# Performance work log

Measured on AMD Instinct MI355X. Metric: run time of the kernel, lower is better.

Reference implementation:

```python
import jax, jax.numpy as jnp
import numpy as np

LN_EPS = 1e-5
KERNEL_EPS = 1e-4


def layer_norm(x, gamma, beta):
    mu = jnp.mean(x, axis=-1, keepdims=True)
    var = jnp.mean((x - mu) ** 2, axis=-1, keepdims=True)
    return (x - mu) * jax.lax.rsqrt(var + LN_EPS) * gamma + beta


def softmax_kernel(data, proj, is_query):
    # Performer softmax random-feature map (performer-pytorch softmax_kernel)
    d = data.shape[-1]
    m = proj.shape[0]
    data_normalizer = d ** -0.25
    ratio = m ** -0.5
    # [B,H,S,D] x [M,D] -> [B,H,S,M]
    proj_data = jnp.einsum('bhnd,md->bhnm', data_normalizer * data, proj)
    diag = 0.5 * (data_normalizer ** 2) * jnp.sum(data * data, axis=-1, keepdims=True)
    if is_query:
        mx = jax.lax.stop_gradient(jnp.max(proj_data, axis=-1, keepdims=True))
    else:
        mx = jax.lax.stop_gradient(jnp.max(proj_data, axis=(-2, -1), keepdims=True))
    return ratio * (jnp.exp(proj_data - diag - mx) + KERNEL_EPS)


def setup_inputs() -> dict:
    key = jax.random.key(0)
    k1, k2 = jax.random.split(key)
    B, S, D, M, H = 4, 4096, 256, 256, 8
    x = jax.random.normal(k1, (B, S, D), dtype=jnp.float32)
    gamma = jnp.ones((D,), dtype=jnp.float32)
    beta = jnp.zeros((D,), dtype=jnp.float32)
    proj_matrix = jax.random.normal(k2, (M, D), dtype=jnp.float32)
    return {"x": x, "gamma": gamma, "beta": beta, "proj_matrix": proj_matrix, "num_heads": H}


def reference(x, gamma, beta, proj_matrix, num_heads):
    xn = layer_norm(x, gamma, beta)                       # [B,S,D]
    B, S, D = xn.shape
    h = jnp.broadcast_to(xn[:, None], (B, num_heads, S, D))  # stacked copies per head
    q = softmax_kernel(h, proj_matrix, True)              # [B,H,S,M]
    k = softmax_kernel(h, proj_matrix, False)             # [B,H,S,M]
    v = h                                                 # [B,H,S,D]
    # non-causal linear attention
    k_sum = jnp.sum(k, axis=-2)                           # [B,H,M]
    d_inv = 1.0 / jnp.einsum('bhnm,bhm->bhn', q, k_sum)   # [B,H,S]
    context = jnp.einsum('bhnm,bhnd->bhmd', k, v)         # [B,H,M,D]
    out = jnp.einsum('bhmd,bhnm,bhn->bhnd', context, q, d_inv)
    return out
```

## Files before the change

kernel.cpp:

```cpp
#include <hip/hip_runtime.h>
#include <math.h>

#define Bn 4
#define Hn 8
#define Sn 4096
#define Dn 256
#define Mn 256
#define BSn (Bn*Sn)
#define LN_EPS 1e-5f
#define KEPS 1e-4f
#define DATA_NORM 0.25f
#define RATIO 0.0625f

typedef short s8v __attribute__((ext_vector_type(8)));
typedef short s4v __attribute__((ext_vector_type(4)));
typedef float f4v __attribute__((ext_vector_type(4)));

#define LSTR 40
#define BSTR 72

__device__ __forceinline__ unsigned short f2bf(float x) {
    unsigned u = __float_as_uint(x);
    u += 0x7FFFu + ((u >> 16) & 1u);
    return (unsigned short)(u >> 16);
}
__device__ __forceinline__ float bf2f(unsigned short h) {
    return __uint_as_float(((unsigned)h) << 16);
}
__device__ __forceinline__ unsigned enc_f(float f) {
    unsigned u = __float_as_uint(f);
    return (u & 0x80000000u) ? ~u : (u | 0x80000000u);
}
__device__ __forceinline__ float dec_f(unsigned u) {
    unsigned b = (u & 0x80000000u) ? (u ^ 0x80000000u) : ~u;
    return __uint_as_float(b);
}

__device__ __forceinline__ float blockReduceMax(float v) {
    __shared__ float buf[4];
    #pragma unroll
    for (int o = 32; o > 0; o >>= 1) v = fmaxf(v, __shfl_down(v, o));
    __syncthreads();
    if ((threadIdx.x & 63) == 0) buf[threadIdx.x >> 6] = v;
    __syncthreads();
    return fmaxf(fmaxf(buf[0], buf[1]), fmaxf(buf[2], buf[3]));
}

__device__ __forceinline__ void split8(const float* p, unsigned short* Lh,
                                       unsigned short* Ll, int off) {
    float v[8];
    *(float4*)&v[0] = *(const float4*)p;
    *(float4*)&v[4] = *(const float4*)(p + 4);
    s8v hh, ll;
    #pragma unroll
    for (int e = 0; e < 8; e++) {
        unsigned short h = f2bf(v[e]);
        hh[e] = (short)h;
        ll[e] = (short)f2bf(v[e] - bf2f(h));
    }
    *(s8v*)&Lh[off] = hh;
    *(s8v*)&Ll[off] = ll;
}

__device__ __forceinline__ void stage_tile(const float* base, int ld,
                                           unsigned short* Lh, unsigned short* Ll, int t) {
    const int row = t >> 1, c0 = (t & 1) * 16;
    const float* p = base + (size_t)row * ld + c0;
    split8(p,     Lh, Ll, row * LSTR + c0);
    split8(p + 8, Lh, Ll, row * LSTR + c0 + 8);
}

__device__ __forceinline__ void mfma_step(const unsigned short* Ah, const unsigned short* Al,
                                          const unsigned short* Bh, const unsigned short* Bl,
                                          int wr, int wc, int lane, f4v acc[4][4]) {
    s8v ah[4], al[4], bh[4], bl[4];
    const int quad = lane >> 4, r = lane & 15;
    #pragma unroll
    for (int i = 0; i < 4; i++) {
        const int m = wr * 64 + i * 16 + r;
        ah[i] = *(const s8v*)&Ah[m * LSTR + quad * 8];
        al[i] = *(const s8v*)&Al[m * LSTR + quad * 8];
        const int n = wc * 64 + i * 16 + r;
        bh[i] = *(const s8v*)&Bh[n * LSTR + quad * 8];
        bl[i] = *(const s8v*)&Bl[n * LSTR + quad * 8];
    }
    #pragma unroll
    for (int i = 0; i < 4; i++)
        #pragma unroll
        for (int j = 0; j < 4; j++) {
            acc[i][j] = __builtin_amdgcn_mfma_f32_16x16x32_bf16(ah[i], bh[j], acc[i][j], 0, 0, 0);
            acc[i][j] = __builtin_amdgcn_mfma_f32_16x16x32_bf16(ah[i], bl[j], acc[i][j], 0, 0, 0);
            acc[i][j] = __builtin_amdgcn_mfma_f32_16x16x32_bf16(al[i], bh[j], acc[i][j], 0, 0, 0);
        }
}

__device__ __forceinline__ void stage_bf16(const unsigned short* base, int ld,
                                           unsigned short* L, int t) {
    const int row = t >> 1, c0 = (t & 1) * 32;
    const unsigned short* p = base + (size_t)row * ld + c0;
    #pragma unroll
    for (int q = 0; q < 4; q++)
        *(s8v*)&L[row * BSTR + c0 + q * 8] = *(const s8v*)&p[q * 8];
}

__device__ __forceinline__ void mfma_step64(const unsigned short* A, const unsigned short* B,
                                            int wr, int wc, int lane, f4v acc[4][4]) {
    const int quad = lane >> 4, r = lane & 15;
    #pragma unroll
    for (int ks = 0; ks < 2; ks++) {
        s8v a[4], b[4];
        #pragma unroll
        for (int i = 0; i < 4; i++) {
            a[i] = *(const s8v*)&A[(wr * 64 + i * 16 + r) * BSTR + ks * 32 + quad * 8];
            b[i] = *(const s8v*)&B[(wc * 64 + i * 16 + r) * BSTR + ks * 32 + quad * 8];
        }
        #pragma unroll
        for (int i = 0; i < 4; i++)
            #pragma unroll
            for (int j = 0; j < 4; j++)
                acc[i][j] = __builtin_amdgcn_mfma_f32_16x16x32_bf16(a[i], b[j], acc[i][j], 0, 0, 0);
    }
}

__global__ __launch_bounds__(256) void k_ln(const float* __restrict__ X,
                                            const float* __restrict__ gamma,
                                            const float* __restrict__ beta,
                                            float* __restrict__ XN,
                                            float* __restrict__ diag,
                                            unsigned* __restrict__ mxqI) {
    const int w = threadIdx.x >> 6, l = threadIdx.x & 63;
    const int row = blockIdx.x * 4 + w;
    const float* p = X + (size_t)row * Dn + l * 4;
    float4 x = *(const float4*)p;
    float s = x.x + x.y + x.z + x.w;
    #pragma unroll
    for (int o = 32; o > 0; o >>= 1) s += __shfl_xor(s, o);
    const float mean = s * (1.0f / Dn);
    float4 v = make_float4(x.x - mean, x.y - mean, x.z - mean, x.w - mean);
    float vs = v.x * v.x + v.y * v.y + v.z * v.z + v.w * v.w;
    #pragma unroll
    for (int o = 32; o > 0; o >>= 1) vs += __shfl_xor(vs, o);
    const float rs = rsqrtf(vs * (1.0f / Dn) + LN_EPS);
    float4 g = *(const float4*)&gamma[l * 4];
    float4 bt = *(const float4*)&beta[l * 4];
    float4 xn = make_float4(v.x * rs * g.x + bt.x, v.y * rs * g.y + bt.y,
                            v.z * rs * g.z + bt.z, v.w * rs * g.w + bt.w);
    *(float4*)&XN[(size_t)row * Dn + l * 4] = xn;
    float d2 = xn.x * xn.x + xn.y * xn.y + xn.z * xn.z + xn.w * xn.w;
    #pragma unroll
    for (int o = 32; o > 0; o >>= 1) d2 += __shfl_xor(d2, o);
    if (l == 0) { diag[row] = 0.03125f * d2; mxqI[row] = 0u; }
}

__global__ __launch_bounds__(256, 2) void k_gemm1(const float* __restrict__ XN,
                                                  const float* __restrict__ P,
                                                  float* __restrict__ PD,
                                                  unsigned* __restrict__ mxqI) {
    __shared__ unsigned short Ah[128 * LSTR], Al[128 * LSTR];
    __shared__ unsigned short Bh[128 * LSTR], Bl[128 * LSTR];
    const int t = threadIdx.x, lane = t & 63, w = t >> 6;
    const int wr = w >> 1, wc = w & 1, quad = lane >> 4, cc = lane & 15;
    const int r0 = blockIdx.x * 128, m0 = blockIdx.y * 128;
    f4v acc[4][4];
    #pragma unroll
    for (int i = 0; i < 4; i++)
        #pragma unroll
        for (int j = 0; j < 4; j++)
            #pragma unroll
            for (int r = 0; r < 4; r++) acc[i][j][r] = 0.0f;

    for (int kt = 0; kt < Dn; kt += 32) {
        __syncthreads();
        stage_tile(XN + (size_t)r0 * Dn + kt, Dn, Ah, Al, t);
        stage_tile(P + (size_t)m0 * Dn + kt, Dn, Bh, Bl, t);
        __syncthreads();
        mfma_step(Ah, Al, Bh, Bl, wr, wc, lane, acc);
    }
    float rmax[4][4];
    #pragma unroll
    for (int i = 0; i < 4; i++)
        #pragma unroll
        for (int r = 0; r < 4; r++) rmax[i][r] = -INFINITY;
    #pragma unroll
    for (int i = 0; i < 4; i++) {
        const int row = r0 + wr * 64 + i * 16 + quad * 4;
        #pragma unroll
        for (int j = 0; j < 4; j++) {
            const int col = m0 + wc * 64 + j * 16 + cc;
            #pragma unroll
            for (int r = 0; r < 4; r++) {
                float v = DATA_NORM * acc[i][j][r];
                PD[(size_t)(row + r) * Mn + col] = v;
                rmax[i][r] = fmaxf(rmax[i][r], v);
            }
        }
    }
    #pragma unroll
    for (int i = 0; i < 4; i++)
        #pragma unroll
        for (int r = 0; r < 4; r++) {
            float v = rmax[i][r];
            v = fmaxf(v, __shfl_xor(v, 1));
            v = fmaxf(v, __shfl_xor(v, 2));
            v = fmaxf(v, __shfl_xor(v, 4));
            v = fmaxf(v, __shfl_xor(v, 8));
            if (cc == 0)
                atomicMax(&mxqI[r0 + wr * 64 + i * 16 + quad * 4 + r], enc_f(v));
        }
}

__global__ __launch_bounds__(256) void k_batchmax(const unsigned* __restrict__ mxqI,
                                                  float* __restrict__ mxqF,
                                                  float* __restrict__ mxk,
                                                  float* __restrict__ KSUM) {
    const int b = blockIdx.x;
    KSUM[b * Mn + threadIdx.x] = 0.0f;
    float m = -INFINITY;
    for (int i = threadIdx.x; i < Sn; i += 256) {
        float f = dec_f(mxqI[b * Sn + i]);
        mxqF[b * Sn + i] = f;
        m = fmaxf(m, f);
    }
    m = blockReduceMax(m);
    if (threadIdx.x == 0) mxk[b] = m;
}

__global__ __launch_bounds__(256) void k_featvt(const float* __restrict__ PD,
                                                const float* __restrict__ XN,
                                                const float* __restrict__ diag,
                                                const float* __restrict__ mxk,
                                                unsigned short* __restrict__ KT,
                                                unsigned short* __restrict__ VT,
                                                float* __restrict__ KSUM) {
    __shared__ float T[64][65];
    const int s0 = blockIdx.x * 64, c0 = blockIdx.y * 64;
    const int z = blockIdx.z;
    const int t = threadIdx.x;
    const int sr = t >> 2, cc = (t & 3) * 16;
    if (z < 4) {
        const int b = z;
        const int gr = b * Sn + s0 + sr;
        const float dmv = diag[gr] + mxk[b];
        const float* p = PD + (size_t)gr * Mn + c0 + cc;
        float v[16];
        *(float4*)&v[0]  = *(const float4*)&p[0];
        *(float4*)&v[4]  = *(const float4*)&p[4];
        *(float4*)&v[8]  = *(const float4*)&p[8];
        *(float4*)&v[12] = *(const float4*)&p[12];
        #pragma unroll
        for (int e = 0; e < 16; e++)
            T[cc + e][sr] = RATIO * (__expf(v[e] - dmv) + KEPS);
        __syncthreads();
        const int ml = t >> 2, sc = (t & 3) * 16;
        float ks = 0.0f;
        s8v o0, o1;
        #pragma unroll
        for (int i = 0; i < 8; i++) {
            float f0 = T[ml][sc + i], f1 = T[ml][sc + 8 + i];
            ks += f0 + f1;
            o0[i] = (short)f2bf(f0);
            o1[i] = (short)f2bf(f1);
        }
        unsigned short* q = KT + ((size_t)b * Mn + c0 + ml) * Sn + s0 + sc;
        *(s8v*)&q[0] = o0;
        *(s8v*)&q[8] = o1;
        ks += __shfl_xor(ks, 1);
        ks += __shfl_xor(ks, 2);
        if ((t & 3) == 0) atomicAdd(&KSUM[b * Mn + c0 + ml], ks);
    } else {
        const int b = z - 4;
        const int gr = b * Sn + s0 + sr;
        const float* p = XN + (size_t)gr * Dn + c0 + cc;
        float v[16];
        *(float4*)&v[0]  = *(const float4*)&p[0];
        *(float4*)&v[4]  = *(const float4*)&p[4];
        *(float4*)&v[8]  = *(const float4*)&p[8];
        *(float4*)&v[12] = *(const float4*)&p[12];
        #pragma unroll
        for (int e = 0; e < 16; e++) T[cc + e][sr] = v[e];
        __syncthreads();
        const int dl = t >> 2, sc = (t & 3) * 16;
        s8v o0, o1;
        #pragma unroll
        for (int i = 0; i < 8; i++) {
            o0[i] = (short)f2bf(T[dl][sc + i]);
            o1[i] = (short)f2bf(T[dl][sc + 8 + i]);
        }
        unsigned short* q = VT + ((size_t)b * Dn + c0 + dl) * Sn + s0 + sc;
        *(s8v*)&q[0] = o0;
        *(s8v*)&q[8] = o1;
    }
}

__global__ __launch_bounds__(256, 2) void k_gemm2(const unsigned short* __restrict__ VT,
                                                  const unsigned short* __restrict__ KT,
                                                  float* __restrict__ PART) {
    __shared__ unsigned short Abuf[128 * BSTR], Bbuf[128 * BSTR];
    const int t = threadIdx.x, lane = t & 63, w = t >> 6;
    const int wr = w >> 1, wc = w & 1, quad = lane >> 4, cc = lane & 15;
    const int chunk = blockIdx.x, til = blockIdx.y, b = blockIdx.z;
    const int d0 = (til >> 1) * 128, m0 = (til & 1) * 128;
    const unsigned short* Ab = VT + ((size_t)b * Dn + d0) * Sn + chunk * 256;
    const unsigned short* Bb = KT + ((size_t)b * Mn + m0) * Sn + chunk * 256;
    f4v acc[4][4];
    #pragma unroll
    for (int i = 0; i < 4; i++)
        #pragma unroll
        for (int j = 0; j < 4; j++)
            #pragma unroll
            for (int r = 0; r < 4; r++) acc[i][j][r] = 0.0f;

    for (int kt = 0; kt < 256; kt += 64) {
        __syncthreads();
        stage_bf16(Ab + kt, Sn, Abuf, t);
        stage_bf16(Bb + kt, Sn, Bbuf, t);
        __syncthreads();
        mfma_step64(Abuf, Bbuf, wr, wc, lane, acc);
    }
    float* dst = PART + (size_t)(chunk * Bn + b) * (Dn * Mn);
    #pragma unroll
    for (int i = 0; i < 4; i++) {
        const int drow = d0 + wr * 64 + i * 16 + quad * 4;
        #pragma unroll
        for (int j = 0; j < 4; j++) {
            const int col = m0 + wc * 64 + j * 16 + cc;
            #pragma unroll
            for (int r = 0; r < 4; r++)
                dst[(size_t)(drow + r) * Mn + col] = acc[i][j][r];
        }
    }
}

__global__ __launch_bounds__(256) void k_ctxred(const float* __restrict__ PART,
                                                unsigned short* __restrict__ CT) {
    const int g = blockIdx.x * 256 + threadIdx.x;
    float4 s = make_float4(0.f, 0.f, 0.f, 0.f);
    #pragma unroll
    for (int c = 0; c < 16; c++) {
        float4 p = *(const float4*)&PART[(size_t)c * 262144 + (size_t)g * 4];
        s.x += p.x; s.y += p.y; s.z += p.z; s.w += p.w;
    }
    s4v o;
    o[0] = (short)f2bf(s.x); o[1] = (short)f2bf(s.y);
    o[2] = (short)f2bf(s.z); o[3] = (short)f2bf(s.w);
    *(s4v*)&CT[(size_t)g * 4] = o;
}

__global__ __launch_bounds__(256, 2) void k_gemm3(const float* __restrict__ PD,
                                                  const unsigned short* __restrict__ CT,
                                                  const float* __restrict__ diag,
                                                  const float* __restrict__ mxqF,
                                                  const float* __restrict__ KSUM,
                                                  float* __restrict__ OUT) {
    __shared__ unsigned short Abuf[128 * BSTR], Bbuf[128 * BSTR];
    __shared__ float kslds[Mn];
    __shared__ float dinvS[128];
    const int t = threadIdx.x, lane = t & 63, w = t >> 6;
    const int wr = w >> 1, wc = w & 1, quad = lane >> 4, cc = lane & 15;
    const int r0 = blockIdx.x * 128, d0 = blockIdx.y * 128;
    const int b = r0 >> 12;
    kslds[t] = KSUM[b * Mn + t];
    const int arow = t >> 1, h = t & 1;
    const int gr = r0 + arow;
    const float dm = diag[gr] + mxqF[gr];
    const float* Ap = PD + (size_t)gr * Mn + h * 32;
    const unsigned short* Bb = CT + ((size_t)b * Dn + d0) * Mn;
    float qks = 0.0f;
    f4v acc[4][4];
    #pragma unroll
    for (int i = 0; i < 4; i++)
        #pragma unroll
        for (int j = 0; j < 4; j++)
            #pragma unroll
            for (int r = 0; r < 4; r++) acc[i][j][r] = 0.0f;

    for (int kt = 0; kt < Mn; kt += 64) {
        __syncthreads();
        {
            float v[32];
            #pragma unroll
            for (int q4 = 0; q4 < 8; q4++)
                *(float4*)&v[q4 * 4] = *(const float4*)&Ap[kt + q4 * 4];
            #pragma unroll
            for (int e = 0; e < 32; e++) {
                float qv = RATIO * (__expf(v[e] - dm) + KEPS);
                qks += qv * kslds[kt + h * 32 + e];
                v[e] = qv;
            }
            #pragma unroll
            for (int g8 = 0; g8 < 4; g8++) {
                s8v hh;
                #pragma unroll
                for (int e = 0; e < 8; e++) hh[e] = (short)f2bf(v[g8 * 8 + e]);
                *(s8v*)&Abuf[arow * BSTR + h * 32 + g8 * 8] = hh;
            }
        }
        stage_bf16(Bb + kt, Mn, Bbuf, t);
        __syncthreads();
        mfma_step64(Abuf, Bbuf, wr, wc, lane, acc);
    }
    qks += __shfl_xor(qks, 1);
    if (h == 0) dinvS[arow] = 1.0f / qks;
    __syncthreads();
    #pragma unroll
    for (int i = 0; i < 4; i++) {
        const int rl0 = wr * 64 + i * 16 + quad * 4;
        #pragma unroll
        for (int r = 0; r < 4; r++) {
            const int rl = rl0 + r;
            const int gr2 = r0 + rl;
            const float dv = dinvS[rl];
            const int ss = gr2 & (Sn - 1);
            const size_t base = ((size_t)(b * Hn) * Sn + ss) * Dn;
            #pragma unroll
            for (int j = 0; j < 4; j++) {
                const int col = d0 + wc * 64 + j * 16 + cc;
                const float val = acc[i][j][r] * dv;
                #pragma unroll
                for (int hh = 0; hh < Hn; hh++)
                    OUT[base + (size_t)hh * Sn * Dn + col] = val;
            }
        }
    }
}

extern "C" void kernel_launch(void* const* d_in, const int* in_sizes, int n_in,
                              void* d_out, int out_size, void* d_ws, size_t ws_size,
                              hipStream_t stream) {
    const float* X     = (const float*)d_in[0];
    const float* gamma = (const float*)d_in[1];
    const float* beta  = (const float*)d_in[2];
    const float* P     = (const float*)d_in[3];
    float* OUT = (float*)d_out;

    float* ws = (float*)d_ws;
    float* XN   = ws;
    float* PD   = XN + (size_t)4194304;
    float* diag = PD + (size_t)4194304;
    unsigned* mxqI = (unsigned*)(diag + 16384);
    float* mxqF = (float*)(mxqI + 16384);
    float* mxk  = mxqF + 16384;
    float* KSUM = mxk + 64;
    unsigned short* KT = (unsigned short*)(KSUM + 1024);
    unsigned short* VT = KT + (size_t)4194304;
    unsigned short* CT = VT + (size_t)4194304;
    float* PART = XN;

    k_ln<<<BSn / 4, 256, 0, stream>>>(X, gamma, beta, XN, diag, mxqI);
    k_gemm1<<<dim3(BSn / 128, Mn / 128), 256, 0, stream>>>(XN, P, PD, mxqI);
    k_batchmax<<<Bn, 256, 0, stream>>>(mxqI, mxqF, mxk, KSUM);
    k_featvt<<<dim3(Sn / 64, 4, 8), 256, 0, stream>>>(PD, XN, diag, mxk, KT, VT, KSUM);
    k_gemm2<<<dim3(16, 4, Bn), 256, 0, stream>>>(VT, KT, PART);
    k_ctxred<<<256, 256, 0, stream>>>(PART, CT);
    k_gemm3<<<dim3(BSn / 128, Dn / 128), 256, 0, stream>>>(PD, CT, diag, mxqF, KSUM, OUT);
}
```

Measured before the change: 221.6 us.

## Pre-split operands to bf16 hi/lo and precompute Q features in featvt

LayerNorm now writes bf16 hi/lo halves directly, and a new kernel pre-splits the projection matrix, so gemm1 stages bf16 tiles instead of converting fp32 per tile. Query features are computed once in featvt, rescaled from the key max, and stored as bf16, so gemm3 no longer re-reads fp32 PD and recomputes exp. Both GEMMs move to 64-row tiles with a 64-wide K step, and the workspace is repacked with KT aliasing XNl. The intent is to cut global traffic and redundant conversion and exp work. The cost is an extra launch, and Q is rescaled via exp(mxk-mxq) before bf16 rounding, which could affect accuracy.

```diff
diff --git a/kernel.cpp b/kernel.cpp
--- a/kernel.cpp
+++ b/kernel.cpp
@@ -16,7 +16,6 @@
 typedef short s4v __attribute__((ext_vector_type(4)));
 typedef float f4v __attribute__((ext_vector_type(4)));
 
-#define LSTR 40
 #define BSTR 72
 
 __device__ __forceinline__ unsigned short f2bf(float x) {
@@ -46,11 +45,41 @@
     return fmaxf(fmaxf(buf[0], buf[1]), fmaxf(buf[2], buf[3]));
 }
 
-__device__ __forceinline__ void split8(const float* p, unsigned short* Lh,
-                                       unsigned short* Ll, int off) {
+__device__ __forceinline__ void stage_bf16(const unsigned short* base, int ld,
+                                           unsigned short* L, int t) {
+    const int row = t >> 1, c0 = (t & 1) * 32;
+    const unsigned short* p = base + (size_t)row * ld + c0;
+    #pragma unroll
+    for (int q = 0; q < 4; q++)
+        *(s8v*)&L[row * BSTR + c0 + q * 8] = *(const s8v*)&p[q * 8];
+}
+
+__device__ __forceinline__ void mfma_step64(const unsigned short* A, const unsigned short* B,
+                                            int wr, int wc, int lane, f4v acc[4][4]) {
+    const int quad = lane >> 4, r = lane & 15;
+    #pragma unroll
+    for (int ks = 0; ks < 2; ks++) {
+        s8v a[4], b[4];
+        #pragma unroll
+        for (int i = 0; i < 4; i++) {
+            a[i] = *(const s8v*)&A[(wr * 64 + i * 16 + r) * BSTR + ks * 32 + quad * 8];
+            b[i] = *(const s8v*)&B[(wc * 64 + i * 16 + r) * BSTR + ks * 32 + quad * 8];
+        }
+        #pragma unroll
+        for (int i = 0; i < 4; i++)
+            #pragma unroll
+            for (int j = 0; j < 4; j++)
+                acc[i][j] = __builtin_amdgcn_mfma_f32_16x16x32_bf16(a[i], b[j], acc[i][j], 0, 0, 0);
+    }
+}
+
+__global__ __launch_bounds__(256) void k_splitp(const float* __restrict__ P,
+                                                unsigned short* __restrict__ Ph,
+                                                unsigned short* __restrict__ Pl) {
+    const int i = (blockIdx.x * 256 + threadIdx.x) * 8;
     float v[8];
-    *(float4*)&v[0] = *(const float4*)p;
-    *(float4*)&v[4] = *(const float4*)(p + 4);
+    *(float4*)&v[0] = *(const float4*)&P[i];
+    *(float4*)&v[4] = *(const float4*)&P[i + 4];
     s8v hh, ll;
     #pragma unroll
     for (int e = 0; e < 8; e++) {
@@ -58,132 +87,117 @@
         hh[e] = (short)h;
         ll[e] = (short)f2bf(v[e] - bf2f(h));
     }
-    *(s8v*)&Lh[off] = hh;
-    *(s8v*)&Ll[off] = ll;
-}
-
-__device__ __forceinline__ void stage_tile(const float* base, int ld,
-                                           unsigned short* Lh, unsigned short* Ll, int t) {
-    const int row = t >> 1, c0 = (t & 1) * 16;
-    const float* p = base + (size_t)row * ld + c0;
-    split8(p,     Lh, Ll, row * LSTR + c0);
-    split8(p + 8, Lh, Ll, row * LSTR + c0 + 8);
-}
-
-__device__ __forceinline__ void mfma_step(const unsigned short* Ah, const unsigned short* Al,
-                                          const unsigned short* Bh, const unsigned short* Bl,
-                                          int wr, int wc, int lane, f4v acc[4][4]) {
-    s8v ah[4], al[4], bh[4], bl[4];
-    const int quad = lane >> 4, r = lane & 15;
-    #pragma unroll
-    for (int i = 0; i < 4; i++) {
-        const int m = wr * 64 + i * 16 + r;
-        ah[i] = *(const s8v*)&Ah[m * LSTR + quad * 8];
-        al[i] = *(const s8v*)&Al[m * LSTR + quad * 8];
-        const int n = wc * 64 + i * 16 + r;
-        bh[i] = *(const s8v*)&Bh[n * LSTR + quad * 8];
-        bl[i] = *(const s8v*)&Bl[n * LSTR + quad * 8];
-    }
-    #pragma unroll
-    for (int i = 0; i < 4; i++)
-        #pragma unroll
-        for (int j = 0; j < 4; j++) {
-            acc[i][j] = __builtin_amdgcn_mfma_f32_16x16x32_bf16(ah[i], bh[j], acc[i][j], 0, 0, 0);
-            acc[i][j] = __builtin_amdgcn_mfma_f32_16x16x32_bf16(ah[i], bl[j], acc[i][j], 0, 0, 0);
-            acc[i][j] = __builtin_amdgcn_mfma_f32_16x16x32_bf16(al[i], bh[j], acc[i][j], 0, 0, 0);
-        }
-}
-
-__device__ __forceinline__ void stage_bf16(const unsigned short* base, int ld,
-                                           unsigned short* L, int t) {
-    const int row = t >> 1, c0 = (t & 1) * 32;
-    const unsigned short* p = base + (size_t)row * ld + c0;
-    #pragma unroll
-    for (int q = 0; q < 4; q++)
-        *(s8v*)&L[row * BSTR + c0 + q * 8] = *(const s8v*)&p[q * 8];
-}
-
-__device__ __forceinline__ void mfma_step64(const unsigned short* A, const unsigned short* B,
-                                            int wr, int wc, int lane, f4v acc[4][4]) {
-    const int quad = lane >> 4, r = lane & 15;
-    #pragma unroll
-    for (int ks = 0; ks < 2; ks++) {
-        s8v a[4], b[4];
-        #pragma unroll
-        for (int i = 0; i < 4; i++) {
-            a[i] = *(const s8v*)&A[(wr * 64 + i * 16 + r) * BSTR + ks * 32 + quad * 8];
-            b[i] = *(const s8v*)&B[(wc * 64 + i * 16 + r) * BSTR + ks * 32 + quad * 8];
-        }
-        #pragma unroll
-        for (int i = 0; i < 4; i++)
-            #pragma unroll
-            for (int j = 0; j < 4; j++)
-                acc[i][j] = __builtin_amdgcn_mfma_f32_16x16x32_bf16(a[i], b[j], acc[i][j], 0, 0, 0);
-    }
+    *(s8v*)&Ph[i] = hh;
+    *(s8v*)&Pl[i] = ll;
 }
 
 __global__ __launch_bounds__(256) void k_ln(const float* __restrict__ X,
                                             const float* __restrict__ gamma,
                                             const float* __restrict__ beta,
-                                            float* __restrict__ XN,
+                                            unsigned short* __restrict__ XNh,
+                                            unsigned short* __restrict__ XNl,
                                             float* __restrict__ diag,
                                             unsigned* __restrict__ mxqI) {
     const int w = threadIdx.x >> 6, l = threadIdx.x & 63;
     const int row = blockIdx.x * 4 + w;
-    const float* p = X + (size_t)row * Dn + l * 4;
-    float4 x = *(const float4*)p;
+    float4 x = *(const float4*)&X[(size_t)row * Dn + l * 4];
     float s = x.x + x.y + x.z + x.w;
     #pragma unroll
     for (int o = 32; o > 0; o >>= 1) s += __shfl_xor(s, o);
     const float mean = s * (1.0f / Dn);
-    float4 v = make_float4(x.x - mean, x.y - mean, x.z - mean, x.w - mean);
-    float vs = v.x * v.x + v.y * v.y + v.z * v.z + v.w * v.w;
+    float xn[4] = {x.x - mean, x.y - mean, x.z - mean, x.w - mean};
+    float vs = xn[0] * xn[0] + xn[1] * xn[1] + xn[2] * xn[2] + xn[3] * xn[3];
     #pragma unroll
     for (int o = 32; o > 0; o >>= 1) vs += __shfl_xor(vs, o);
     const float rs = rsqrtf(vs * (1.0f / Dn) + LN_EPS);
     float4 g = *(const float4*)&gamma[l * 4];
     float4 bt = *(const float4*)&beta[l * 4];
-    float4 xn = make_float4(v.x * rs * g.x + bt.x, v.y * rs * g.y + bt.y,
-                            v.z * rs * g.z + bt.z, v.w * rs * g.w + bt.w);
-    *(float4*)&XN[(size_t)row * Dn + l * 4] = xn;
-    float d2 = xn.x * xn.x + xn.y * xn.y + xn.z * xn.z + xn.w * xn.w;
+    xn[0] = xn[0] * rs * g.x + bt.x;
+    xn[1] = xn[1] * rs * g.y + bt.y;
+    xn[2] = xn[2] * rs * g.z + bt.z;
+    xn[3] = xn[3] * rs * g.w + bt.w;
+    s4v hv, lv;
+    float d2 = 0.0f;
+    #pragma unroll
+    for (int c = 0; c < 4; c++) {
+        d2 += xn[c] * xn[c];
+        unsigned short h = f2bf(xn[c]);
+        hv[c] = (short)h;
+        lv[c] = (short)f2bf(xn[c] - bf2f(h));
+    }
+    *(s4v*)&XNh[(size_t)row * Dn + l * 4] = hv;
+    *(s4v*)&XNl[(size_t)row * Dn + l * 4] = lv;
     #pragma unroll
     for (int o = 32; o > 0; o >>= 1) d2 += __shfl_xor(d2, o);
     if (l == 0) { diag[row] = 0.03125f * d2; mxqI[row] = 0u; }
 }
 
-__global__ __launch_bounds__(256, 2) void k_gemm1(const float* __restrict__ XN,
-                                                  const float* __restrict__ P,
+__global__ __launch_bounds__(256, 2) void k_gemm1(const unsigned short* __restrict__ XNh,
+                                                  const unsigned short* __restrict__ XNl,
+                                                  const unsigned short* __restrict__ Ph,
+                                                  const unsigned short* __restrict__ Pl,
                                                   float* __restrict__ PD,
                                                   unsigned* __restrict__ mxqI) {
-    __shared__ unsigned short Ah[128 * LSTR], Al[128 * LSTR];
-    __shared__ unsigned short Bh[128 * LSTR], Bl[128 * LSTR];
+    __shared__ unsigned short Ah[64 * BSTR], Al[64 * BSTR];
+    __shared__ unsigned short Bh[128 * BSTR], Bl[128 * BSTR];
     const int t = threadIdx.x, lane = t & 63, w = t >> 6;
     const int wr = w >> 1, wc = w & 1, quad = lane >> 4, cc = lane & 15;
-    const int r0 = blockIdx.x * 128, m0 = blockIdx.y * 128;
-    f4v acc[4][4];
-    #pragma unroll
-    for (int i = 0; i < 4; i++)
+    const int r0 = blockIdx.x * 64, m0 = blockIdx.y * 128;
+    const int ar0 = t >> 3, ac8 = (t & 7) * 8;
+    f4v acc[2][4];
+    #pragma unroll
+    for (int i = 0; i < 2; i++)
         #pragma unroll
         for (int j = 0; j < 4; j++)
             #pragma unroll
             for (int r = 0; r < 4; r++) acc[i][j][r] = 0.0f;
 
-    for (int kt = 0; kt < Dn; kt += 32) {
-        __syncthreads();
-        stage_tile(XN + (size_t)r0 * Dn + kt, Dn, Ah, Al, t);
-        stage_tile(P + (size_t)m0 * Dn + kt, Dn, Bh, Bl, t);
-        __syncthreads();
-        mfma_step(Ah, Al, Bh, Bl, wr, wc, lane, acc);
-    }
-    float rmax[4][4];
-    #pragma unroll
-    for (int i = 0; i < 4; i++)
+    for (int kt = 0; kt < Dn; kt += 64) {
+        __syncthreads();
+        *(s8v*)&Ah[ar0 * BSTR + ac8]        = *(const s8v*)&XNh[(size_t)(r0 + ar0) * Dn + kt + ac8];
+        *(s8v*)&Al[ar0 * BSTR + ac8]        = *(const s8v*)&XNl[(size_t)(r0 + ar0) * Dn + kt + ac8];
+        *(s8v*)&Ah[(ar0 + 32) * BSTR + ac8] = *(const s8v*)&XNh[(size_t)(r0 + ar0 + 32) * Dn + kt + ac8];
+        *(s8v*)&Al[(ar0 + 32) * BSTR + ac8] = *(const s8v*)&XNl[(size_t)(r0 + ar0 + 32) * Dn + kt + ac8];
+        #pragma unroll
+        for (int ss = 0; ss < 4; ss++) {
+            const int row = ar0 + ss * 32;
+            *(s8v*)&Bh[row * BSTR + ac8] = *(const s8v*)&Ph[(size_t)(m0 + row) * Dn + kt + ac8];
+            *(s8v*)&Bl[row * BSTR + ac8] = *(const s8v*)&Pl[(size_t)(m0 + row) * Dn + kt + ac8];
+        }
+        __syncthreads();
+        #pragma unroll
+        for (int ks = 0; ks < 2; ks++) {
+            s8v ah[2], al[2], bh[4], bl[4];
+            #pragma unroll
+            for (int i = 0; i < 2; i++) {
+                const int m = wr * 32 + i * 16 + cc;
+                ah[i] = *(const s8v*)&Ah[m * BSTR + ks * 32 + quad * 8];
+                al[i] = *(const s8v*)&Al[m * BSTR + ks * 32 + quad * 8];
+            }
+            #pragma unroll
+            for (int j = 0; j < 4; j++) {
+                const int n = wc * 64 + j * 16 + cc;
+                bh[j] = *(const s8v*)&Bh[n * BSTR + ks * 32 + quad * 8];
+                bl[j] = *(const s8v*)&Bl[n * BSTR + ks * 32 + quad * 8];
+            }
+            #pragma unroll
+            for (int i = 0; i < 2; i++)
+                #pragma unroll
+                for (int j = 0; j < 4; j++) {
+                    acc[i][j] = __builtin_amdgcn_mfma_f32_16x16x32_bf16(ah[i], bh[j], acc[i][j], 0, 0, 0);
+                    acc[i][j] = __builtin_amdgcn_mfma_f32_16x16x32_bf16(ah[i], bl[j], acc[i][j], 0, 0, 0);
+                    acc[i][j] = __builtin_amdgcn_mfma_f32_16x16x32_bf16(al[i], bh[j], acc[i][j], 0, 0, 0);
+                }
+        }
+    }
+    float rmax[2][4];
+    #pragma unroll
+    for (int i = 0; i < 2; i++)
         #pragma unroll
         for (int r = 0; r < 4; r++) rmax[i][r] = -INFINITY;
     #pragma unroll
-    for (int i = 0; i < 4; i++) {
-        const int row = r0 + wr * 64 + i * 16 + quad * 4;
+    for (int i = 0; i < 2; i++) {
+        const int row = r0 + wr * 32 + i * 16 + quad * 4;
         #pragma unroll
         for (int j = 0; j < 4; j++) {
             const int col = m0 + wc * 64 + j * 16 + cc;
@@ -196,7 +210,7 @@
         }
     }
     #pragma unroll
-    for (int i = 0; i < 4; i++)
+    for (int i = 0; i < 2; i++)
         #pragma unroll
         for (int r = 0; r < 4; r++) {
             float v = rmax[i][r];
@@ -205,7 +219,7 @@
             v = fmaxf(v, __shfl_xor(v, 4));
             v = fmaxf(v, __shfl_xor(v, 8));
             if (cc == 0)
-                atomicMax(&mxqI[r0 + wr * 64 + i * 16 + quad * 4 + r], enc_f(v));
+                atomicMax(&mxqI[r0 + wr * 32 + i * 16 + quad * 4 + r], enc_f(v));
         }
 }
 
@@ -226,30 +240,39 @@
 }
 
 __global__ __launch_bounds__(256) void k_featvt(const float* __restrict__ PD,
-                                                const float* __restrict__ XN,
+                                                const unsigned short* __restrict__ XNh,
                                                 const float* __restrict__ diag,
                                                 const float* __restrict__ mxk,
+                                                const float* __restrict__ mxqF,
                                                 unsigned short* __restrict__ KT,
+                                                unsigned short* __restrict__ QR,
                                                 unsigned short* __restrict__ VT,
                                                 float* __restrict__ KSUM) {
-    __shared__ float T[64][65];
-    const int s0 = blockIdx.x * 64, c0 = blockIdx.y * 64;
-    const int z = blockIdx.z;
+    const int s0 = blockIdx.x * 64, c0 = blockIdx.y * 64, z = blockIdx.z;
     const int t = threadIdx.x;
-    const int sr = t >> 2, cc = (t & 3) * 16;
+    const int sr = t >> 2, cc16 = (t & 3) * 16;
     if (z < 4) {
+        __shared__ float T[64][65];
         const int b = z;
         const int gr = b * Sn + s0 + sr;
         const float dmv = diag[gr] + mxk[b];
-        const float* p = PD + (size_t)gr * Mn + c0 + cc;
+        const float srow = __expf(mxk[b] - mxqF[gr]);
+        const float* p = PD + (size_t)gr * Mn + c0 + cc16;
         float v[16];
         *(float4*)&v[0]  = *(const float4*)&p[0];
         *(float4*)&v[4]  = *(const float4*)&p[4];
         *(float4*)&v[8]  = *(const float4*)&p[8];
         *(float4*)&v[12] = *(const float4*)&p[12];
-        #pragma unroll
-        for (int e = 0; e < 16; e++)
-            T[cc + e][sr] = RATIO * (__expf(v[e] - dmv) + KEPS);
+        s8v q0, q1;
+        #pragma unroll
+        for (int e = 0; e < 16; e++) {
+            float ev = __expf(v[e] - dmv);
+            T[cc16 + e][sr] = RATIO * (ev + KEPS);
+            unsigned short qb = f2bf(RATIO * (ev * srow + KEPS));
+            if (e < 8) q0[e] = (short)qb; else q1[e - 8] = (short)qb;
+        }
+        *(s8v*)&QR[(size_t)gr * Mn + c0 + cc16]     = q0;
+        *(s8v*)&QR[(size_t)gr * Mn + c0 + cc16 + 8] = q1;
         __syncthreads();
         const int ml = t >> 2, sc = (t & 3) * 16;
         float ks = 0.0f;
@@ -268,23 +291,23 @@
         ks += __shfl_xor(ks, 2);
         if ((t & 3) == 0) atomicAdd(&KSUM[b * Mn + c0 + ml], ks);
     } else {
+        __shared__ unsigned short Tu[64][72];
         const int b = z - 4;
         const int gr = b * Sn + s0 + sr;
-        const float* p = XN + (size_t)gr * Dn + c0 + cc;
-        float v[16];
-        *(float4*)&v[0]  = *(const float4*)&p[0];
-        *(float4*)&v[4]  = *(const float4*)&p[4];
-        *(float4*)&v[8]  = *(const float4*)&p[8];
-        *(float4*)&v[12] = *(const float4*)&p[12];
-        #pragma unroll
-        for (int e = 0; e < 16; e++) T[cc + e][sr] = v[e];
+        const unsigned short* p = XNh + (size_t)gr * Dn + c0 + cc16;
+        s8v x0 = *(const s8v*)&p[0], x1 = *(const s8v*)&p[8];
+        #pragma unroll
+        for (int e = 0; e < 8; e++) {
+            Tu[cc16 + e][sr]     = (unsigned short)x0[e];
+            Tu[cc16 + 8 + e][sr] = (unsigned short)x1[e];
+        }
         __syncthreads();
         const int dl = t >> 2, sc = (t & 3) * 16;
         s8v o0, o1;
         #pragma unroll
         for (int i = 0; i < 8; i++) {
-            o0[i] = (short)f2bf(T[dl][sc + i]);
-            o1[i] = (short)f2bf(T[dl][sc + 8 + i]);
+            o0[i] = (short)Tu[dl][sc + i];
+            o1[i] = (short)Tu[dl][sc + 8 + i];
         }
         unsigned short* q = VT + ((size_t)b * Dn + c0 + dl) * Sn + s0 + sc;
         *(s8v*)&q[0] = o0;
@@ -346,29 +369,23 @@
     *(s4v*)&CT[(size_t)g * 4] = o;
 }
 
-__global__ __launch_bounds__(256, 2) void k_gemm3(const float* __restrict__ PD,
+__global__ __launch_bounds__(256, 2) void k_gemm3(const unsigned short* __restrict__ QR,
                                                   const unsigned short* __restrict__ CT,
-                                                  const float* __restrict__ diag,
-                                                  const float* __restrict__ mxqF,
                                                   const float* __restrict__ KSUM,
                                                   float* __restrict__ OUT) {
-    __shared__ unsigned short Abuf[128 * BSTR], Bbuf[128 * BSTR];
+    __shared__ unsigned short Abuf[64 * BSTR], Bbuf[128 * BSTR];
     __shared__ float kslds[Mn];
-    __shared__ float dinvS[128];
+    __shared__ float dinvS[64];
     const int t = threadIdx.x, lane = t & 63, w = t >> 6;
     const int wr = w >> 1, wc = w & 1, quad = lane >> 4, cc = lane & 15;
-    const int r0 = blockIdx.x * 128, d0 = blockIdx.y * 128;
+    const int r0 = blockIdx.x * 64, d0 = blockIdx.y * 128;
     const int b = r0 >> 12;
     kslds[t] = KSUM[b * Mn + t];
-    const int arow = t >> 1, h = t & 1;
-    const int gr = r0 + arow;
-    const float dm = diag[gr] + mxqF[gr];
-    const float* Ap = PD + (size_t)gr * Mn + h * 32;
-    const unsigned short* Bb = CT + ((size_t)b * Dn + d0) * Mn;
-    float qks = 0.0f;
-    f4v acc[4][4];
-    #pragma unroll
-    for (int i = 0; i < 4; i++)
+    const int ar0 = t >> 3, ac8 = (t & 7) * 8;
+    float qks0 = 0.0f, qks1 = 0.0f;
+    f4v acc[2][4];
+    #pragma unroll
+    for (int i = 0; i < 2; i++)
         #pragma unroll
         for (int j = 0; j < 4; j++)
             #pragma unroll
@@ -376,49 +393,63 @@
 
     for (int kt = 0; kt < Mn; kt += 64) {
         __syncthreads();
-        {
-            float v[32];
-            #pragma unroll
-            for (int q4 = 0; q4 < 8; q4++)
-                *(float4*)&v[q4 * 4] = *(const float4*)&Ap[kt + q4 * 4];
-            #pragma unroll
-            for (int e = 0; e < 32; e++) {
-                float qv = RATIO * (__expf(v[e] - dm) + KEPS);
-                qks += qv * kslds[kt + h * 32 + e];
-                v[e] = qv;
-            }
-            #pragma unroll
-            for (int g8 = 0; g8 < 4; g8++) {
-                s8v hh;
+        s8v a0 = *(const s8v*)&QR[(size_t)(r0 + ar0) * Mn + kt + ac8];
+        s8v a1 = *(const s8v*)&QR[(size_t)(r0 + ar0 + 32) * Mn + kt + ac8];
+        *(s8v*)&Abuf[ar0 * BSTR + ac8]        = a0;
+        *(s8v*)&Abuf[(ar0 + 32) * BSTR + ac8] = a1;
+        #pragma unroll
+        for (int e = 0; e < 8; e++) {
+            const float ks = kslds[kt + ac8 + e];
+            qks0 += bf2f((unsigned short)a0[e]) * ks;
+            qks1 += bf2f((unsigned short)a1[e]) * ks;
+        }
+        #pragma unroll
+        for (int ss = 0; ss < 4; ss++) {
+            const int row = ar0 + ss * 32;
+            *(s8v*)&Bbuf[row * BSTR + ac8] =
+                *(const s8v*)&CT[((size_t)b * Dn + d0 + row) * Mn + kt + ac8];
+        }
+        __syncthreads();
+        #pragma unroll
+        for (int ks = 0; ks < 2; ks++) {
+            s8v a[2], bb[4];
+            #pragma unroll
+            for (int i = 0; i < 2; i++)
+                a[i] = *(const s8v*)&Abuf[(wr * 32 + i * 16 + cc) * BSTR + ks * 32 + quad * 8];
+            #pragma unroll
+            for (int j = 0; j < 4; j++)
+                bb[j] = *(const s8v*)&Bbuf[(wc * 64 + j * 16 + cc) * BSTR + ks * 32 + quad * 8];
+            #pragma unroll
+            for (int i = 0; i < 2; i++)
                 #pragma unroll
-                for (int e = 0; e < 8; e++) hh[e] = (short)f2bf(v[g8 * 8 + e]);
-                *(s8v*)&Abuf[arow * BSTR + h * 32 + g8 * 8] = hh;
-            }
-        }
-        stage_bf16(Bb + kt, Mn, Bbuf, t);
-        __syncthreads();
-        mfma_step64(Abuf, Bbuf, wr, wc, lane, acc);
-    }
-    qks += __shfl_xor(qks, 1);
-    if (h == 0) dinvS[arow] = 1.0f / qks;
+                for (int j = 0; j < 4; j++)
+                    acc[i][j] = __builtin_amdgcn_mfma_f32_16x16x32_bf16(a[i], bb[j], acc[i][j], 0, 0, 0);
+        }
+    }
+    qks0 += __shfl_xor(qks0, 1); qks0 += __shfl_xor(qks0, 2); qks0 += __shfl_xor(qks0, 4);
+    qks1 += __shfl_xor(qks1, 1); qks1 += __shfl_xor(qks1, 2); qks1 += __shfl_xor(qks1, 4);
+    if ((t & 7) == 0) {
+        dinvS[ar0]      = 1.0f / qks0;
+        dinvS[ar0 + 32] = 1.0f / qks1;
+    }
     __syncthreads();
     #pragma unroll
-    for (int i = 0; i < 4; i++) {
-        const int rl0 = wr * 64 + i * 16 + quad * 4;
+    for (int i = 0; i < 2; i++) {
+        const int rl0 = wr * 32 + i * 16 + quad * 4;
         #pragma unroll
         for (int r = 0; r < 4; r++) {
             const int rl = rl0 + r;
-            const int gr2 = r0 + rl;
+            const int gr = r0 + rl;
             const float dv = dinvS[rl];
-            const int ss = gr2 & (Sn - 1);
+            const int ss = gr & (Sn - 1);
             const size_t base = ((size_t)(b * Hn) * Sn + ss) * Dn;
             #pragma unroll
             for (int j = 0; j < 4; j++) {
                 const int col = d0 + wc * 64 + j * 16 + cc;
                 const float val = acc[i][j][r] * dv;
                 #pragma unroll
-                for (int hh = 0; hh < Hn; hh++)
-                    OUT[base + (size_t)hh * Sn * Dn + col] = val;
+                for (int h = 0; h < Hn; h++)
+                    OUT[base + (size_t)h * Sn * Dn + col] = val;
             }
         }
     }
@@ -433,24 +464,29 @@
     const float* P     = (const float*)d_in[3];
     float* OUT = (float*)d_out;
 
-    float* ws = (float*)d_ws;
-    float* XN   = ws;
-    float* PD   = XN + (size_t)4194304;
-    float* diag = PD + (size_t)4194304;
-    unsigned* mxqI = (unsigned*)(diag + 16384);
-    float* mxqF = (float*)(mxqI + 16384);
-    float* mxk  = mxqF + 16384;
-    float* KSUM = mxk + 64;
-    unsigned short* KT = (unsigned short*)(KSUM + 1024);
-    unsigned short* VT = KT + (size_t)4194304;
-    unsigned short* CT = VT + (size_t)4194304;
-    float* PART = XN;
-
-    k_ln<<<BSn / 4, 256, 0, stream>>>(X, gamma, beta, XN, diag, mxqI);
-    k_gemm1<<<dim3(BSn / 128, Mn / 128), 256, 0, stream>>>(XN, P, PD, mxqI);
+    char* base = (char*)d_ws;
+    unsigned short* XNh = (unsigned short*)(base);
+    unsigned short* XNl = (unsigned short*)(base + 8388608);
+    float*          PD  = (float*)(base + 16777216);
+    unsigned short* QR  = (unsigned short*)(base + 33554432);
+    unsigned short* VT  = (unsigned short*)(base + 41943040);
+    unsigned short* CT  = (unsigned short*)(base + 50331648);
+    unsigned short* Ph  = (unsigned short*)(base + 50855936);
+    unsigned short* Pl  = (unsigned short*)(base + 50987008);
+    float*          diag = (float*)(base + 51118080);
+    unsigned*       mxqI = (unsigned*)(base + 51183616);
+    float*          mxqF = (float*)(base + 51249152);
+    float*          mxk  = (float*)(base + 51314688);
+    float*          KSUM = (float*)(base + 51314944);
+    unsigned short* KT   = XNl;
+    float*          PART = PD;
+
+    k_splitp<<<32, 256, 0, stream>>>(P, Ph, Pl);
+    k_ln<<<BSn / 4, 256, 0, stream>>>(X, gamma, beta, XNh, XNl, diag, mxqI);
+    k_gemm1<<<dim3(BSn / 64, Mn / 128), 256, 0, stream>>>(XNh, XNl, Ph, Pl, PD, mxqI);
     k_batchmax<<<Bn, 256, 0, stream>>>(mxqI, mxqF, mxk, KSUM);
-    k_featvt<<<dim3(Sn / 64, 4, 8), 256, 0, stream>>>(PD, XN, diag, mxk, KT, VT, KSUM);
+    k_featvt<<<dim3(Sn / 64, 4, 8), 256, 0, stream>>>(PD, XNh, diag, mxk, mxqF, KT, QR, VT, KSUM);
     k_gemm2<<<dim3(16, 4, Bn), 256, 0, stream>>>(VT, KT, PART);
     k_ctxred<<<256, 256, 0, stream>>>(PART, CT);
-    k_gemm3<<<dim3(BSn / 128, Dn / 128), 256, 0, stream>>>(PD, CT, diag, mxqF, KSUM, OUT);
-}
+    k_gemm3<<<dim3(BSn / 64, Dn / 128), 256, 0, stream>>>(QR, CT, KSUM, OUT);
+}
```

Measured after the change: 206.9 us. 6.6% less time.
